# Performance work log

Hardware: AMD Instinct MI355X
Metric: run time of the kernel (lower is better)

The kernel has to match this reference:

```python
import jax, jax.numpy as jnp
import numpy as np

HIDDEN = 1024
N_HEAD = 16
HEAD_DIM = HIDDEN // N_HEAD


def setup_inputs() -> dict:
    key = jax.random.key(0)
    ks = jax.random.split(key, 11)
    B, S, D, H, E = 4, 1024, HIDDEN, N_HEAD, HEAD_DIM
    sc = 0.02
    return {
        "query": jax.random.normal(ks[0], (B, S, D), jnp.float32),
        "key": jax.random.normal(ks[1], (B, S, D), jnp.float32),
        "value": jax.random.normal(ks[2], (B, S, D), jnp.float32),
        # per-head projection weights stacked over heads (torch Linear: y = x @ W.T + b)
        "Wq": jax.random.normal(ks[3], (H, D, E), jnp.float32) * sc,
        "bq": jax.random.normal(ks[4], (H, E), jnp.float32) * sc,
        "Wk": jax.random.normal(ks[5], (H, D, E), jnp.float32) * sc,
        "bk": jax.random.normal(ks[6], (H, E), jnp.float32) * sc,
        "Wv": jax.random.normal(ks[7], (H, D, E), jnp.float32) * sc,
        "bv": jax.random.normal(ks[8], (H, E), jnp.float32) * sc,
        "Wo": jax.random.normal(ks[9], (D, D), jnp.float32) * sc,
        "bo": jax.random.normal(ks[10], (D,), jnp.float32) * sc,
    }


def reference(query, key, value, Wq, bq, Wk, bk, Wv, bv, Wo, bo):
    B, S, D = query.shape
    H, _, E = Wq.shape
    # per-head linear projections (vectorized over heads)
    q = jnp.einsum("bsd,hde->bhse", query, Wq) + bq[None, :, None, :]
    k = jnp.einsum("bsd,hde->bhse", key, Wk) + bk[None, :, None, :]
    v = jnp.einsum("bsd,hde->bhse", value, Wv) + bv[None, :, None, :]
    scale = jnp.sqrt(jnp.asarray(E, q.dtype))
    scores = jnp.einsum("bhse,bhte->bhst", q, k) / scale  # [B,H,S,S]
    attn = jax.nn.softmax(scores, axis=-1)  # dropout is identity in eval
    wv = jnp.einsum("bhst,bhte->bhse", attn, v)  # [B,H,S,E]
    # concat heads along feature dim (head h -> slice h*E:(h+1)*E)
    wv = wv.transpose(0, 2, 1, 3).reshape(B, S, H * E)
    out = wv @ Wo.T + bo  # final linear; output dropout identity in eval
    return out
```

## Files before the change

kernel.cpp:

```cpp
#include <hip/hip_runtime.h>

typedef unsigned short u16;
typedef unsigned int u32;
typedef __attribute__((ext_vector_type(8))) short bf16x8;
typedef __attribute__((ext_vector_type(4))) float f32x4;

#define B_SZ 4
#define S_SZ 1024
#define D_SZ 1024
#define H_SZ 16
#define E_SZ 64
#define M_SZ (B_SZ * S_SZ)

__device__ __forceinline__ u16 f2bf(float f) {
  union { float f; unsigned u; } x; x.f = f;
  unsigned r = (x.u + 0x7FFFu + ((x.u >> 16) & 1u)) >> 16;
  return (u16)r;
}

__device__ __forceinline__ u32 pack_bf16(float lo, float hi) {
  return (u32)f2bf(lo) | ((u32)f2bf(hi) << 16);
}

__device__ __forceinline__ void async16(const void* g, void* l) {
  __builtin_amdgcn_global_load_lds(
      (const __attribute__((address_space(1))) void*)g,
      (__attribute__((address_space(3))) void*)l, 16, 0, 0);
}

__device__ __forceinline__ f32x4 mfma16(bf16x8 a, bf16x8 b, f32x4 c) {
  return __builtin_amdgcn_mfma_f32_16x16x32_bf16(a, b, c, 0, 0, 0);
}

__global__ void prep(const float* __restrict__ q, const float* __restrict__ k,
                     const float* __restrict__ v, const float* __restrict__ Wo,
                     const float* __restrict__ Wq, const float* __restrict__ Wk,
                     const float* __restrict__ Wv,
                     u16* __restrict__ oq, u16* __restrict__ ok,
                     u16* __restrict__ ov, u16* __restrict__ oWo,
                     u16* __restrict__ Tq, u16* __restrict__ Tk, u16* __restrict__ Tv) {
  __shared__ float tile[64 * 68];
  const int tid = threadIdx.x;
  if (blockIdx.x < 6656) {
    int gid = blockIdx.x * 256 + tid;
    const float* in;
    u16* out;
    int i;
    if (gid < (3 << 19)) {
      int sel = gid >> 19;
      i = (gid & ((1 << 19) - 1)) << 3;
      in = sel == 0 ? q : (sel == 1 ? k : v);
      out = sel == 0 ? oq : (sel == 1 ? ok : ov);
    } else {
      i = (gid - (3 << 19)) << 3;
      in = Wo;
      out = oWo;
    }
    float4 a = *(const float4*)(in + i);
    float4 b = *(const float4*)(in + i + 4);
    alignas(16) u16 r[8];
    r[0] = f2bf(a.x); r[1] = f2bf(a.y); r[2] = f2bf(a.z); r[3] = f2bf(a.w);
    r[4] = f2bf(b.x); r[5] = f2bf(b.y); r[6] = f2bf(b.z); r[7] = f2bf(b.w);
    *(uint4*)(out + i) = *(uint4*)r;
  } else {
    const int blk = blockIdx.x - 6656;
    const int wsel = blk >> 8;
    const int bi = blk & 255;
    const float* W = wsel == 0 ? Wq : (wsel == 1 ? Wk : Wv);
    u16* WT = wsel == 0 ? Tq : (wsel == 1 ? Tk : Tv);
    const int h = bi >> 4;
    const int d0 = (bi & 15) << 6;
#pragma unroll
    for (int c = 0; c < 4; ++c) {
      const int dd = c * 16 + (tid >> 4);
      const int e4 = (tid & 15) << 2;
      float4 vq = *(const float4*)(W + (h << 16) + ((d0 + dd) << 6) + e4);
      *(float4*)(tile + dd * 68 + e4) = vq;
    }
    __syncthreads();
    {
      const int e = tid >> 2;
      const int dc = (tid & 3) << 4;
      alignas(16) u16 outv[16];
#pragma unroll
      for (int i = 0; i < 16; ++i) outv[i] = f2bf(tile[(dc + i) * 68 + e]);
      u16* dst = WT + (((size_t)(h << 6) + e) << 10) + d0 + dc;
      *(uint4*)(dst) = *(uint4*)outv;
      *(uint4*)(dst + 8) = *(uint4*)(outv + 8);
    }
  }
}

__global__ __launch_bounds__(256)
void gemm3(const u16* __restrict__ qb, const u16* __restrict__ kb, const u16* __restrict__ vb,
           const u16* __restrict__ Tq, const u16* __restrict__ Tk, const u16* __restrict__ Tv,
           const float* __restrict__ bq, const float* __restrict__ bk, const float* __restrict__ bv,
           u16* __restrict__ Qp, u16* __restrict__ Kp, u16* __restrict__ VpT) {
  __shared__ u16 Al[128 * 64];
  __shared__ u16 Bl[128 * 64];
  const int wg = blockIdx.x;
  const int swz = (wg & 7) * 96 + (wg >> 3);
  const int g = swz >> 8;
  const int bi = swz & 255;
  const u16* A = g == 0 ? qb : (g == 1 ? kb : vb);
  const u16* BT = g == 0 ? Tq : (g == 1 ? Tk : Tv);
  const float* bias = g == 0 ? bq : (g == 1 ? bk : bv);
  u16* Cout = g == 0 ? Qp : (g == 1 ? Kp : VpT);
  const float scale = g == 0 ? 0.125f : 1.0f;

  const int tid = threadIdx.x;
  const int wave = tid >> 6;
  const int lane = tid & 63;
  const int l15 = lane & 15, lq = lane >> 4;
  const int bm = bi >> 3;
  const int bn = bi & 7;
  const int row0 = bm << 7, col0 = bn << 7;
  const int wr = ((wave >> 1) & 1) << 6;
  const int wc = (wave & 1) << 6;

  f32x4 acc[4][4];
#pragma unroll
  for (int m = 0; m < 4; ++m)
#pragma unroll
    for (int n = 0; n < 4; ++n) acc[m][n] = (f32x4)0.0f;

  for (int k0 = 0; k0 < 1024; k0 += 64) {
    __syncthreads();
#pragma unroll
    for (int c = 0; c < 4; ++c) {
      const int x = c * 4096 + tid * 16;
      const int gx = x ^ (((x >> 7) & 7) << 4);
      const int row = gx >> 7;
      const int cb = gx & 127;
      const u16* ga = A + (size_t)(row0 + row) * 1024 + k0 + (cb >> 1);
      const u16* gb = BT + (size_t)(col0 + row) * 1024 + k0 + (cb >> 1);
      async16(ga, (char*)Al + x);
      async16(gb, (char*)Bl + x);
    }
    __syncthreads();

    bf16x8 af[4][2], bfr[4][2];
#pragma unroll
    for (int m = 0; m < 4; ++m)
#pragma unroll
      for (int kf = 0; kf < 2; ++kf) {
        int r = wr + m * 16 + l15;
        int byte = ((r << 7) + kf * 64 + lq * 16) ^ ((r & 7) << 4);
        af[m][kf] = *(const bf16x8*)((const char*)Al + byte);
      }
#pragma unroll
    for (int n = 0; n < 4; ++n)
#pragma unroll
      for (int kf = 0; kf < 2; ++kf) {
        int r = wc + n * 16 + l15;
        int byte = ((r << 7) + kf * 64 + lq * 16) ^ ((r & 7) << 4);
        bfr[n][kf] = *(const bf16x8*)((const char*)Bl + byte);
      }
    if (g == 2) {
#pragma unroll
      for (int kf = 0; kf < 2; ++kf)
#pragma unroll
        for (int m = 0; m < 4; ++m)
#pragma unroll
          for (int n = 0; n < 4; ++n)
            acc[m][n] = mfma16(af[m][kf], bfr[n][kf], acc[m][n]);
    } else {
#pragma unroll
      for (int kf = 0; kf < 2; ++kf)
#pragma unroll
        for (int m = 0; m < 4; ++m)
#pragma unroll
          for (int n = 0; n < 4; ++n)
            acc[m][n] = mfma16(bfr[n][kf], af[m][kf], acc[m][n]);
    }
  }

  if (g == 2) {
#pragma unroll
    for (int m = 0; m < 4; ++m)
#pragma unroll
      for (int n = 0; n < 4; ++n) {
        int col = col0 + wc + n * 16 + l15;
        float bv = bias[col];
        int rowb = row0 + wr + m * 16 + lq * 4;
        alignas(8) u16 r4[4];
#pragma unroll
        for (int j = 0; j < 4; ++j) r4[j] = f2bf(acc[m][n][j] + bv);
        *(uint2*)(Cout + (size_t)col * 4096 + rowb) = *(uint2*)r4;
      }
  } else {
    float4 b4[4];
#pragma unroll
    for (int n = 0; n < 4; ++n)
      b4[n] = *(const float4*)(bias + col0 + wc + n * 16 + lq * 4);
#pragma unroll
    for (int m = 0; m < 4; ++m) {
      int row = row0 + wr + m * 16 + l15;
#pragma unroll
      for (int n = 0; n < 4; ++n) {
        int colbase = col0 + wc + n * 16 + lq * 4;
        u32 lo = pack_bf16((acc[m][n][0] + b4[n].x) * scale,
                           (acc[m][n][1] + b4[n].y) * scale);
        u32 hi = pack_bf16((acc[m][n][2] + b4[n].z) * scale,
                           (acc[m][n][3] + b4[n].w) * scale);
        uint2 wv; wv.x = lo; wv.y = hi;
        *(uint2*)(Cout + (size_t)row * 1024 + colbase) = wv;
      }
    }
  }
}

__global__ __launch_bounds__(512, 4)
void gemmO8(const u16* __restrict__ A, const u16* __restrict__ BT,
            const float* __restrict__ bias, float* __restrict__ out) {
  __shared__ u16 Al[2][128 * 64];
  __shared__ u16 Bl[2][128 * 64];
  const int tid = threadIdx.x;
  const int wave = tid >> 6;
  const int lane = tid & 63;
  const int l15 = lane & 15, lq = lane >> 4;
  const int wg = blockIdx.x;
  const int bi = (wg & 7) * 32 + (wg >> 3);
  const int bm = bi >> 3;
  const int bn = bi & 7;
  const int row0 = bm << 7, col0 = bn << 7;
  const int wr = (wave >> 1) << 5;
  const int wc = (wave & 1) << 6;

  int xs[2], rowS[2], cbS[2];
#pragma unroll
  for (int c = 0; c < 2; ++c) {
    int x = c * 8192 + tid * 16;
    int gx = x ^ (((x >> 7) & 7) << 4);
    xs[c] = x;
    rowS[c] = gx >> 7;
    cbS[c] = (gx & 127) >> 1;
  }

  f32x4 acc[2][4];
#pragma unroll
  for (int m = 0; m < 2; ++m)
#pragma unroll
    for (int n = 0; n < 4; ++n) acc[m][n] = (f32x4)0.0f;

#pragma unroll
  for (int c = 0; c < 2; ++c) {
    async16(A + (size_t)(row0 + rowS[c]) * 1024 + cbS[c], (char*)Al[0] + xs[c]);
    async16(BT + (size_t)(col0 + rowS[c]) * 1024 + cbS[c], (char*)Bl[0] + xs[c]);
  }
  __syncthreads();

  int buf = 0;
  for (int k0 = 0; k0 < 1024; k0 += 64) {
    if (k0 + 64 < 1024) {
      const int kn = k0 + 64;
#pragma unroll
      for (int c = 0; c < 2; ++c) {
        async16(A + (size_t)(row0 + rowS[c]) * 1024 + kn + cbS[c], (char*)Al[buf ^ 1] + xs[c]);
        async16(BT + (size_t)(col0 + rowS[c]) * 1024 + kn + cbS[c], (char*)Bl[buf ^ 1] + xs[c]);
      }
    }

    bf16x8 af[2][2], bfr[4][2];
#pragma unroll
    for (int m = 0; m < 2; ++m)
#pragma unroll
      for (int kf = 0; kf < 2; ++kf) {
        int r = wr + m * 16 + l15;
        int byte = ((r << 7) + kf * 64 + lq * 16) ^ ((r & 7) << 4);
        af[m][kf] = *(const bf16x8*)((const char*)Al[buf] + byte);
      }
#pragma unroll
    for (int n = 0; n < 4; ++n)
#pragma unroll
      for (int kf = 0; kf < 2; ++kf) {
        int r = wc + n * 16 + l15;
        int byte = ((r << 7) + kf * 64 + lq * 16) ^ ((r & 7) << 4);
        bfr[n][kf] = *(const bf16x8*)((const char*)Bl[buf] + byte);
      }
#pragma unroll
    for (int kf = 0; kf < 2; ++kf)
#pragma unroll
      for (int m = 0; m < 2; ++m)
#pragma unroll
        for (int n = 0; n < 4; ++n)
          acc[m][n] = mfma16(bfr[n][kf], af[m][kf], acc[m][n]);

    __syncthreads();
    buf ^= 1;
  }

  float4 b4[4];
#pragma unroll
  for (int n = 0; n < 4; ++n)
    b4[n] = *(const float4*)(bias + col0 + wc + n * 16 + lq * 4);
#pragma unroll
  for (int m = 0; m < 2; ++m) {
    int row = row0 + wr + m * 16 + l15;
#pragma unroll
    for (int n = 0; n < 4; ++n) {
      int colbase = col0 + wc + n * 16 + lq * 4;
      float4 v;
      v.x = acc[m][n][0] + b4[n].x;
      v.y = acc[m][n][1] + b4[n].y;
      v.z = acc[m][n][2] + b4[n].z;
      v.w = acc[m][n][3] + b4[n].w;
      *(float4*)(out + (size_t)row * 1024 + colbase) = v;
    }
  }
}

__global__ __launch_bounds__(256)
void attn(const u16* __restrict__ Qp, const u16* __restrict__ Kp,
          const u16* __restrict__ VpT, u16* __restrict__ Ow) {
  __shared__ alignas(16) u16 Kl[2][64 * 64];
  __shared__ alignas(16) u16 VTl[2][64 * 64];
  __shared__ alignas(16) u16 Pl[4][2][16 * 64];
  const int tid = threadIdx.x;
  const int wave = tid >> 6;
  const int lane = tid & 63;
  const int l15 = lane & 15, lq = lane >> 4;
  const int wg = blockIdx.x;
  const int swz = (wg & 7) * 64 + (wg >> 3);
  const int qt = swz & 7;
  const int bh = swz >> 3;
  const int b = bh >> 4, h = bh & 15;
  const size_t bS = (size_t)b * S_SZ;

  const int xs0 = tid * 16, xs1 = 4096 + tid * 16;
  const int r0 = xs0 >> 7, r1 = xs1 >> 7;
  const int c0 = ((xs0 & 127) ^ (((xs0 >> 7) & 7) << 4)) >> 1;
  const int c1 = ((xs1 & 127) ^ (((xs1 >> 7) & 7) << 4)) >> 1;
  const u16* Kb0 = Kp + ((bS + r0) << 10) + h * 64 + c0;
  const u16* Kb1 = Kp + ((bS + r1) << 10) + h * 64 + c1;
  const u16* Vb0 = VpT + (size_t)(h * 64 + r0) * 4096 + bS + c0;
  const u16* Vb1 = VpT + (size_t)(h * 64 + r1) * 4096 + bS + c1;

  bf16x8 aq0[2], aq1[2];
  {
    const u16* qp0 = Qp + ((bS + qt * 128 + wave * 32 + l15) << 10) + h * 64 + lq * 8;
    aq0[0] = *(const bf16x8*)(qp0);
    aq0[1] = *(const bf16x8*)(qp0 + 32);
    const u16* qp1 = qp0 + (16 << 10);
    aq1[0] = *(const bf16x8*)(qp1);
    aq1[1] = *(const bf16x8*)(qp1 + 32);
  }

  f32x4 o0[4], o1[4];
#pragma unroll
  for (int n = 0; n < 4; ++n) { o0[n] = (f32x4)0.0f; o1[n] = (f32x4)0.0f; }
  float m0 = -1e30f, m1 = -1e30f;
  float l0 = 0.f, l1 = 0.f;
  u16* Pw0 = Pl[wave][0];
  u16* Pw1 = Pl[wave][1];

  async16(Kb0, (char*)Kl[0] + xs0);
  async16(Kb1, (char*)Kl[0] + xs1);
  async16(Vb0, (char*)VTl[0] + xs0);
  async16(Vb1, (char*)VTl[0] + xs1);
  __syncthreads();

  int buf = 0;
  for (int t0 = 0; t0 < S_SZ; t0 += 64) {
    if (t0 + 64 < S_SZ) {
      const int tn = t0 + 64;
      async16(Kb0 + ((size_t)tn << 10), (char*)Kl[buf ^ 1] + xs0);
      async16(Kb1 + ((size_t)tn << 10), (char*)Kl[buf ^ 1] + xs1);
      async16(Vb0 + tn, (char*)VTl[buf ^ 1] + xs0);
      async16(Vb1 + tn, (char*)VTl[buf ^ 1] + xs1);
    }

    f32x4 s0[4], s1[4];
#pragma unroll
    for (int n = 0; n < 4; ++n) { s0[n] = (f32x4)0.0f; s1[n] = (f32x4)0.0f; }
    __builtin_amdgcn_s_setprio(1);
#pragma unroll
    for (int n = 0; n < 4; ++n)
#pragma unroll
      for (int kf = 0; kf < 2; ++kf) {
        int r = n * 16 + l15;
        int byte = ((r << 7) + kf * 64 + lq * 16) ^ ((r & 7) << 4);
        bf16x8 bk = *(const bf16x8*)((const char*)Kl[buf] + byte);
        s0[n] = mfma16(bk, aq0[kf], s0[n]);
        s1[n] = mfma16(bk, aq1[kf], s1[n]);
      }
    __builtin_amdgcn_s_setprio(0);

    {
      float mx = s0[0][0];
#pragma unroll
      for (int n = 0; n < 4; ++n)
#pragma unroll
        for (int j = 0; j < 4; ++j) mx = fmaxf(mx, s0[n][j]);
      mx = fmaxf(mx, __shfl_xor(mx, 16, 64));
      mx = fmaxf(mx, __shfl_xor(mx, 32, 64));
      if (__any(mx > m0 + 8.0f)) {
        float mn = fmaxf(m0, mx);
        float alpha = __expf(m0 - mn);
        m0 = mn;
        l0 *= alpha;
        float a0 = __shfl(alpha, lq * 4 + 0, 64);
        float a1 = __shfl(alpha, lq * 4 + 1, 64);
        float a2 = __shfl(alpha, lq * 4 + 2, 64);
        float a3 = __shfl(alpha, lq * 4 + 3, 64);
#pragma unroll
        for (int n = 0; n < 4; ++n) {
          o0[n][0] *= a0; o0[n][1] *= a1; o0[n][2] *= a2; o0[n][3] *= a3;
        }
      }
      float rs = 0.f;
#pragma unroll
      for (int n = 0; n < 4; ++n) {
        float p0 = __expf(s0[n][0] - m0);
        float p1 = __expf(s0[n][1] - m0);
        float p2 = __expf(s0[n][2] - m0);
        float p3 = __expf(s0[n][3] - m0);
        rs += (p0 + p1) + (p2 + p3);
        u32 lo = pack_bf16(p0, p1);
        u32 hi = pack_bf16(p2, p3);
        int byte = (l15 << 7) + (((n * 32 + lq * 8)) ^ ((l15 & 7) << 4));
        uint2 wv; wv.x = lo; wv.y = hi;
        *(uint2*)((char*)Pw0 + byte) = wv;
      }
      rs += __shfl_xor(rs, 16, 64);
      rs += __shfl_xor(rs, 32, 64);
      l0 += rs;
    }
    {
      float mx = s1[0][0];
#pragma unroll
      for (int n = 0; n < 4; ++n)
#pragma unroll
        for (int j = 0; j < 4; ++j) mx = fmaxf(mx, s1[n][j]);
      mx = fmaxf(mx, __shfl_xor(mx, 16, 64));
      mx = fmaxf(mx, __shfl_xor(mx, 32, 64));
      if (__any(mx > m1 + 8.0f)) {
        float mn = fmaxf(m1, mx);
        float alpha = __expf(m1 - mn);
        m1 = mn;
        l1 *= alpha;
        float a0 = __shfl(alpha, lq * 4 + 0, 64);
        float a1 = __shfl(alpha, lq * 4 + 1, 64);
        float a2 = __shfl(alpha, lq * 4 + 2, 64);
        float a3 = __shfl(alpha, lq * 4 + 3, 64);
#pragma unroll
        for (int n = 0; n < 4; ++n) {
          o1[n][0] *= a0; o1[n][1] *= a1; o1[n][2] *= a2; o1[n][3] *= a3;
        }
      }
      float rs = 0.f;
#pragma unroll
      for (int n = 0; n < 4; ++n) {
        float p0 = __expf(s1[n][0] - m1);
        float p1 = __expf(s1[n][1] - m1);
        float p2 = __expf(s1[n][2] - m1);
        float p3 = __expf(s1[n][3] - m1);
        rs += (p0 + p1) + (p2 + p3);
        u32 lo = pack_bf16(p0, p1);
        u32 hi = pack_bf16(p2, p3);
        int byte = (l15 << 7) + (((n * 32 + lq * 8)) ^ ((l15 & 7) << 4));
        uint2 wv; wv.x = lo; wv.y = hi;
        *(uint2*)((char*)Pw1 + byte) = wv;
      }
      rs += __shfl_xor(rs, 16, 64);
      rs += __shfl_xor(rs, 32, 64);
      l1 += rs;
    }

    __builtin_amdgcn_s_setprio(1);
#pragma unroll
    for (int kf = 0; kf < 2; ++kf) {
      int pbyte = (l15 << 7) + ((kf * 64 + lq * 16) ^ ((l15 & 7) << 4));
      bf16x8 pa0 = *(const bf16x8*)((const char*)Pw0 + pbyte);
      bf16x8 pa1 = *(const bf16x8*)((const char*)Pw1 + pbyte);
#pragma unroll
      for (int n = 0; n < 4; ++n) {
        int vr = n * 16 + l15;
        int byte = ((vr << 7) + kf * 64 + lq * 16) ^ ((vr & 7) << 4);
        bf16x8 bv = *(const bf16x8*)((const char*)VTl[buf] + byte);
        o0[n] = mfma16(pa0, bv, o0[n]);
        o1[n] = mfma16(pa1, bv, o1[n]);
      }
    }
    __builtin_amdgcn_s_setprio(0);

    __syncthreads();
    buf ^= 1;
  }

#pragma unroll
  for (int qg = 0; qg < 2; ++qg) {
    float lr = qg == 0 ? l0 : l1;
    f32x4* o = qg == 0 ? o0 : o1;
    float li0 = __shfl(lr, lq * 4 + 0, 64);
    float li1 = __shfl(lr, lq * 4 + 1, 64);
    float li2 = __shfl(lr, lq * 4 + 2, 64);
    float li3 = __shfl(lr, lq * 4 + 3, 64);
    float inv0 = 1.0f / li0, inv1 = 1.0f / li1, inv2 = 1.0f / li2, inv3 = 1.0f / li3;
#pragma unroll
    for (int n = 0; n < 4; ++n) {
      float vals[4] = {o[n][0] * inv0, o[n][1] * inv1, o[n][2] * inv2, o[n][3] * inv3};
#pragma unroll
      for (int j = 0; j < 4; ++j) {
        int row = qt * 128 + wave * 32 + qg * 16 + lq * 4 + j;
        int col = h * 64 + n * 16 + l15;
        Ow[((bS + row) << 10) + col] = f2bf(vals[j]);
      }
    }
  }
}

extern "C" void kernel_launch(void* const* d_in, const int* in_sizes, int n_in,
                              void* d_out, int out_size, void* d_ws, size_t ws_size,
                              hipStream_t stream) {
  const float* q  = (const float*)d_in[0];
  const float* k  = (const float*)d_in[1];
  const float* v  = (const float*)d_in[2];
  const float* Wq = (const float*)d_in[3];
  const float* bq = (const float*)d_in[4];
  const float* Wk = (const float*)d_in[5];
  const float* bk = (const float*)d_in[6];
  const float* Wv = (const float*)d_in[7];
  const float* bv = (const float*)d_in[8];
  const float* Wo = (const float*)d_in[9];
  const float* bo = (const float*)d_in[10];

  char* w = (char*)d_ws;
  const size_t MB = 1u << 20;
  u16* qb  = (u16*)(w + 0 * MB);
  u16* kb  = (u16*)(w + 8 * MB);
  u16* vb  = (u16*)(w + 16 * MB);
  u16* WqT = (u16*)(w + 24 * MB);
  u16* WkT = (u16*)(w + 26 * MB);
  u16* WvT = (u16*)(w + 28 * MB);
  u16* Wob = (u16*)(w + 30 * MB);
  u16* Qp  = (u16*)(w + 32 * MB);
  u16* Kp  = (u16*)(w + 40 * MB);
  u16* VpT = (u16*)(w + 48 * MB);
  u16* wvb = (u16*)(w + 56 * MB);

  prep<<<7424, 256, 0, stream>>>(q, k, v, Wo, Wq, Wk, Wv,
                                 qb, kb, vb, Wob, WqT, WkT, WvT);

  gemm3<<<768, 256, 0, stream>>>(qb, kb, vb, WqT, WkT, WvT, bq, bk, bv, Qp, Kp, VpT);

  attn<<<512, 256, 0, stream>>>(Qp, Kp, VpT, wvb);

  gemmO8<<<256, 512, 0, stream>>>(wvb, Wob, bo, (float*)d_out);
}
```

Measured before the change: 120.6 us.

## Rewrite QKV projection GEMM with 256x256 tiles and double-buffered 8-wave pipeline

The QKV projection kernel now uses 256x256 output tiles per 512-thread block, with double-buffered LDS. Global-to-LDS async loads are interleaved between four MFMA phases, separated by explicit barriers and vmcnt waits. The goal is to hide load latency behind matrix work and raise operand reuse per LDS byte. The trade-off is a smaller grid of 192 blocks, which may leave some compute units idle, plus heavier LDS and register use. The remaining edits in the attention kernel only rename a loop variable.

```diff
diff --git a/kernel.cpp b/kernel.cpp
--- a/kernel.cpp
+++ b/kernel.cpp
@@ -11,6 +11,7 @@
 #define H_SZ 16
 #define E_SZ 64
 #define M_SZ (B_SZ * S_SZ)
+#define NT 16
 
 __device__ __forceinline__ u16 f2bf(float f) {
   union { float f; unsigned u; } x; x.f = f;
@@ -31,6 +32,10 @@
 __device__ __forceinline__ f32x4 mfma16(bf16x8 a, bf16x8 b, f32x4 c) {
   return __builtin_amdgcn_mfma_f32_16x16x32_bf16(a, b, c, 0, 0, 0);
 }
+
+#define BARM asm volatile("s_barrier" ::: "memory")
+#define VMW4 asm volatile("s_waitcnt vmcnt(4)" ::: "memory")
+#define VMW0 asm volatile("s_waitcnt vmcnt(0)" ::: "memory")
 
 __global__ void prep(const float* __restrict__ q, const float* __restrict__ k,
                      const float* __restrict__ v, const float* __restrict__ Wo,
@@ -91,17 +96,25 @@
   }
 }
 
-__global__ __launch_bounds__(256)
+#define STAGE_T(Ml, Moff, t, h)                                                        \
+  do {                                                                                 \
+    async16(Moff + ((h) * 128 + 0) * 1024 + (t) * 64,                                  \
+            (char*)Ml[(t) & 1] + (h) * 16384 + 0 * 8192 + x0);                         \
+    async16(Moff + ((h) * 128 + 64) * 1024 + (t) * 64,                                 \
+            (char*)Ml[(t) & 1] + (h) * 16384 + 1 * 8192 + x0);                         \
+  } while (0)
+
+__global__ __launch_bounds__(512, 2)
 void gemm3(const u16* __restrict__ qb, const u16* __restrict__ kb, const u16* __restrict__ vb,
            const u16* __restrict__ Tq, const u16* __restrict__ Tk, const u16* __restrict__ Tv,
            const float* __restrict__ bq, const float* __restrict__ bk, const float* __restrict__ bv,
            u16* __restrict__ Qp, u16* __restrict__ Kp, u16* __restrict__ VpT) {
-  __shared__ u16 Al[128 * 64];
-  __shared__ u16 Bl[128 * 64];
+  __shared__ u16 Al[2][256 * 64];
+  __shared__ u16 Bl[2][256 * 64];
   const int wg = blockIdx.x;
-  const int swz = (wg & 7) * 96 + (wg >> 3);
-  const int g = swz >> 8;
-  const int bi = swz & 255;
+  const int swz = (wg & 7) * 24 + (wg >> 3);
+  const int g = swz >> 6;
+  const int bi = swz & 63;
   const u16* A = g == 0 ? qb : (g == 1 ? kb : vb);
   const u16* BT = g == 0 ? Tq : (g == 1 ? Tk : Tv);
   const float* bias = g == 0 ? bq : (g == 1 ? bk : bv);
@@ -112,77 +125,140 @@
   const int wave = tid >> 6;
   const int lane = tid & 63;
   const int l15 = lane & 15, lq = lane >> 4;
-  const int bm = bi >> 3;
-  const int bn = bi & 7;
-  const int row0 = bm << 7, col0 = bn << 7;
-  const int wr = ((wave >> 1) & 1) << 6;
-  const int wc = (wave & 1) << 6;
-
-  f32x4 acc[4][4];
-#pragma unroll
-  for (int m = 0; m < 4; ++m)
+  const int bm = bi >> 2, bn = bi & 3;
+  const int row0 = bm << 8, col0 = bn << 8;
+  const int wm = wave >> 2, wn = wave & 3;
+
+  const int x0 = tid * 16;
+  const int sw = ((x0 >> 7) & 7) << 4;
+  const int gx0 = x0 ^ sw;
+  const int srow = gx0 >> 7;
+  const int selem = (gx0 & 127) >> 1;
+  const u16* Aoff = A + (size_t)(row0 + srow) * 1024 + selem;
+  const u16* Boff = BT + (size_t)(col0 + srow) * 1024 + selem;
+
+  f32x4 acc[8][4];
+#pragma unroll
+  for (int m = 0; m < 8; ++m)
 #pragma unroll
     for (int n = 0; n < 4; ++n) acc[m][n] = (f32x4)0.0f;
 
-  for (int k0 = 0; k0 < 1024; k0 += 64) {
-    __syncthreads();
-#pragma unroll
-    for (int c = 0; c < 4; ++c) {
-      const int x = c * 4096 + tid * 16;
-      const int gx = x ^ (((x >> 7) & 7) << 4);
-      const int row = gx >> 7;
-      const int cb = gx & 127;
-      const u16* ga = A + (size_t)(row0 + row) * 1024 + k0 + (cb >> 1);
-      const u16* gb = BT + (size_t)(col0 + row) * 1024 + k0 + (cb >> 1);
-      async16(ga, (char*)Al + x);
-      async16(gb, (char*)Bl + x);
-    }
-    __syncthreads();
-
-    bf16x8 af[4][2], bfr[4][2];
-#pragma unroll
-    for (int m = 0; m < 4; ++m)
-#pragma unroll
-      for (int kf = 0; kf < 2; ++kf) {
-        int r = wr + m * 16 + l15;
-        int byte = ((r << 7) + kf * 64 + lq * 16) ^ ((r & 7) << 4);
-        af[m][kf] = *(const bf16x8*)((const char*)Al + byte);
-      }
-#pragma unroll
-    for (int n = 0; n < 4; ++n)
-#pragma unroll
-      for (int kf = 0; kf < 2; ++kf) {
-        int r = wc + n * 16 + l15;
-        int byte = ((r << 7) + kf * 64 + lq * 16) ^ ((r & 7) << 4);
-        bfr[n][kf] = *(const bf16x8*)((const char*)Bl + byte);
-      }
-    if (g == 2) {
-#pragma unroll
-      for (int kf = 0; kf < 2; ++kf)
-#pragma unroll
-        for (int m = 0; m < 4; ++m)
-#pragma unroll
-          for (int n = 0; n < 4; ++n)
-            acc[m][n] = mfma16(af[m][kf], bfr[n][kf], acc[m][n]);
-    } else {
-#pragma unroll
-      for (int kf = 0; kf < 2; ++kf)
-#pragma unroll
-        for (int m = 0; m < 4; ++m)
-#pragma unroll
-          for (int n = 0; n < 4; ++n)
-            acc[m][n] = mfma16(bfr[n][kf], af[m][kf], acc[m][n]);
-    }
+  STAGE_T(Bl, Boff, 0, 0);
+  STAGE_T(Al, Aoff, 0, 0);
+  STAGE_T(Al, Aoff, 0, 1);
+  STAGE_T(Bl, Boff, 0, 1);
+  STAGE_T(Bl, Boff, 1, 0);
+  STAGE_T(Al, Aoff, 1, 0);
+  VMW4;
+  BARM;
+
+  bf16x8 af[4][2], bf[4][2];
+
+#pragma unroll 1
+  for (int t = 0; t < NT; ++t) {
+    const int b = t & 1;
+
+#pragma unroll
+    for (int i = 0; i < 4; ++i)
+#pragma unroll
+      for (int kk = 0; kk < 2; ++kk) {
+        int r = wm * 128 + i * 16 + l15;
+        af[i][kk] = *(const bf16x8*)((const char*)Al[b] +
+                     ((r << 7) + ((kk * 64 + lq * 16) ^ ((r & 7) << 4))));
+      }
+#pragma unroll
+    for (int j = 0; j < 2; ++j)
+#pragma unroll
+      for (int kk = 0; kk < 2; ++kk) {
+        int rc = wn * 64 + j * 16 + l15;
+        bf[j][kk] = *(const bf16x8*)((const char*)Bl[b] +
+                     ((rc << 7) + ((kk * 64 + lq * 16) ^ ((rc & 7) << 4))));
+      }
+    if (t + 1 < NT) STAGE_T(Al, Aoff, t + 1, 1);
+    BARM;
+    __builtin_amdgcn_s_setprio(1);
+#pragma unroll
+    for (int kk = 0; kk < 2; ++kk)
+#pragma unroll
+      for (int i = 0; i < 4; ++i)
+#pragma unroll
+        for (int j = 0; j < 2; ++j)
+          acc[i][j] = (g == 2) ? mfma16(af[i][kk], bf[j][kk], acc[i][j])
+                               : mfma16(bf[j][kk], af[i][kk], acc[i][j]);
+    __builtin_amdgcn_s_setprio(0);
+    BARM;
+
+#pragma unroll
+    for (int j = 0; j < 2; ++j)
+#pragma unroll
+      for (int kk = 0; kk < 2; ++kk) {
+        int rc = wn * 64 + (2 + j) * 16 + l15;
+        bf[2 + j][kk] = *(const bf16x8*)((const char*)Bl[b] +
+                         ((rc << 7) + ((kk * 64 + lq * 16) ^ ((rc & 7) << 4))));
+      }
+    if (t + 1 < NT) STAGE_T(Bl, Boff, t + 1, 1);
+    BARM;
+    __builtin_amdgcn_s_setprio(1);
+#pragma unroll
+    for (int kk = 0; kk < 2; ++kk)
+#pragma unroll
+      for (int i = 0; i < 4; ++i)
+#pragma unroll
+        for (int j = 0; j < 2; ++j)
+          acc[i][2 + j] = (g == 2) ? mfma16(af[i][kk], bf[2 + j][kk], acc[i][2 + j])
+                                   : mfma16(bf[2 + j][kk], af[i][kk], acc[i][2 + j]);
+    __builtin_amdgcn_s_setprio(0);
+    BARM;
+
+#pragma unroll
+    for (int i = 0; i < 4; ++i)
+#pragma unroll
+      for (int kk = 0; kk < 2; ++kk) {
+        int r = wm * 128 + (4 + i) * 16 + l15;
+        af[i][kk] = *(const bf16x8*)((const char*)Al[b] +
+                     ((r << 7) + ((kk * 64 + lq * 16) ^ ((r & 7) << 4))));
+      }
+    if (t + 2 < NT) STAGE_T(Bl, Boff, t + 2, 0);
+    BARM;
+    __builtin_amdgcn_s_setprio(1);
+#pragma unroll
+    for (int kk = 0; kk < 2; ++kk)
+#pragma unroll
+      for (int i = 0; i < 4; ++i)
+#pragma unroll
+        for (int j = 0; j < 2; ++j)
+          acc[4 + i][j] = (g == 2) ? mfma16(af[i][kk], bf[j][kk], acc[4 + i][j])
+                                   : mfma16(bf[j][kk], af[i][kk], acc[4 + i][j]);
+    __builtin_amdgcn_s_setprio(0);
+    BARM;
+
+    if (t + 2 < NT) STAGE_T(Al, Aoff, t + 2, 0);
+    BARM;
+    __builtin_amdgcn_s_setprio(1);
+#pragma unroll
+    for (int kk = 0; kk < 2; ++kk)
+#pragma unroll
+      for (int i = 0; i < 4; ++i)
+#pragma unroll
+        for (int j = 0; j < 2; ++j)
+          acc[4 + i][2 + j] = (g == 2) ? mfma16(af[i][kk], bf[2 + j][kk], acc[4 + i][2 + j])
+                                       : mfma16(bf[2 + j][kk], af[i][kk], acc[4 + i][2 + j]);
+    __builtin_amdgcn_s_setprio(0);
+
+    if (t < NT - 1) {
+      if (t < NT - 2) { VMW4; } else { VMW0; }
+    }
+    BARM;
   }
 
   if (g == 2) {
 #pragma unroll
-    for (int m = 0; m < 4; ++m)
+    for (int m = 0; m < 8; ++m)
 #pragma unroll
       for (int n = 0; n < 4; ++n) {
-        int col = col0 + wc + n * 16 + l15;
+        int col = col0 + wn * 64 + n * 16 + l15;
         float bv = bias[col];
-        int rowb = row0 + wr + m * 16 + lq * 4;
+        int rowb = row0 + wm * 128 + m * 16 + lq * 4;
         alignas(8) u16 r4[4];
 #pragma unroll
         for (int j = 0; j < 4; ++j) r4[j] = f2bf(acc[m][n][j] + bv);
@@ -192,13 +268,13 @@
     float4 b4[4];
 #pragma unroll
     for (int n = 0; n < 4; ++n)
-      b4[n] = *(const float4*)(bias + col0 + wc + n * 16 + lq * 4);
-#pragma unroll
-    for (int m = 0; m < 4; ++m) {
-      int row = row0 + wr + m * 16 + l15;
+      b4[n] = *(const float4*)(bias + col0 + wn * 64 + n * 16 + lq * 4);
+#pragma unroll
+    for (int m = 0; m < 8; ++m) {
+      int row = row0 + wm * 128 + m * 16 + l15;
 #pragma unroll
       for (int n = 0; n < 4; ++n) {
-        int colbase = col0 + wc + n * 16 + lq * 4;
+        int colbase = col0 + wn * 64 + n * 16 + lq * 4;
         u32 lo = pack_bf16((acc[m][n][0] + b4[n].x) * scale,
                            (acc[m][n][1] + b4[n].y) * scale);
         u32 hi = pack_bf16((acc[m][n][2] + b4[n].z) * scale,
@@ -377,12 +453,12 @@
 #pragma unroll
     for (int n = 0; n < 4; ++n)
 #pragma unroll
-      for (int kf = 0; kf < 2; ++kf) {
+      for (int kk = 0; kk < 2; ++kk) {
         int r = n * 16 + l15;
-        int byte = ((r << 7) + kf * 64 + lq * 16) ^ ((r & 7) << 4);
+        int byte = ((r << 7) + kk * 64 + lq * 16) ^ ((r & 7) << 4);
         bf16x8 bk = *(const bf16x8*)((const char*)Kl[buf] + byte);
-        s0[n] = mfma16(bk, aq0[kf], s0[n]);
-        s1[n] = mfma16(bk, aq1[kf], s1[n]);
+        s0[n] = mfma16(bk, aq0[kk], s0[n]);
+        s1[n] = mfma16(bk, aq1[kk], s1[n]);
       }
     __builtin_amdgcn_s_setprio(0);
 
@@ -469,14 +545,14 @@
 
     __builtin_amdgcn_s_setprio(1);
 #pragma unroll
-    for (int kf = 0; kf < 2; ++kf) {
-      int pbyte = (l15 << 7) + ((kf * 64 + lq * 16) ^ ((l15 & 7) << 4));
+    for (int kk = 0; kk < 2; ++kk) {
+      int pbyte = (l15 << 7) + ((kk * 64 + lq * 16) ^ ((l15 & 7) << 4));
       bf16x8 pa0 = *(const bf16x8*)((const char*)Pw0 + pbyte);
       bf16x8 pa1 = *(const bf16x8*)((const char*)Pw1 + pbyte);
 #pragma unroll
       for (int n = 0; n < 4; ++n) {
         int vr = n * 16 + l15;
-        int byte = ((vr << 7) + kf * 64 + lq * 16) ^ ((vr & 7) << 4);
+        int byte = ((vr << 7) + kk * 64 + lq * 16) ^ ((vr & 7) << 4);
         bf16x8 bv = *(const bf16x8*)((const char*)VTl[buf] + byte);
         o0[n] = mfma16(pa0, bv, o0[n]);
         o1[n] = mfma16(pa1, bv, o1[n]);
@@ -542,7 +618,7 @@
   prep<<<7424, 256, 0, stream>>>(q, k, v, Wo, Wq, Wk, Wv,
                                  qb, kb, vb, Wob, WqT, WkT, WvT);
 
-  gemm3<<<768, 256, 0, stream>>>(qb, kb, vb, WqT, WkT, WvT, bq, bk, bv, Qp, Kp, VpT);
+  gemm3<<<192, 512, 0, stream>>>(qb, kb, vb, WqT, WkT, WvT, bq, bk, bv, Qp, Kp, VpT);
 
   attn<<<512, 256, 0, stream>>>(Qp, Kp, VpT, wvb);
 
```

New measurement: 130.8 us. 1.08x slower.
